# Optimization experiments

Hardware: AMD Instinct MI355X
Metric: run time of the kernel (lower is better)

The kernel has to match this reference:

```python
import jax, jax.numpy as jnp
import numpy as np

BATCH = 16384
INPUT_DIM = 1024
OUTPUT_DIM = 256
SCALES = 5  # pywt level = SCALES - 1

# pywt db4 decomposition low-pass filter (ascending index order)
DB4_LO = jnp.array([
    -0.010597401785069032, 0.0328830116668852, 0.030841381835560764,
    -0.18703481171909309, -0.027983769416859854, 0.6308807679298589,
    0.7148465705529157, 0.2303778133088965], dtype=jnp.float32)
# QMF: dec_hi[k] = (-1)^(k+1) * dec_lo[L-1-k]  (matches pywt sign convention)
_SIGNS = jnp.array([-1.0, 1.0, -1.0, 1.0, -1.0, 1.0, -1.0, 1.0], dtype=jnp.float32)
DB4_HI = DB4_LO[::-1] * _SIGNS


def _dwt_step(x, lo, hi):
    """Single-level pywt dwt with 'symmetric' mode along the last axis.
    x: [B, N] -> (cA, cD) each [B, floor((N+L-1)/2)]."""
    L = lo.shape[0]
    left = x[:, L - 2::-1]          # symmetric (half-point) left extension, L-1 samples
    right = x[:, -1:-L:-1]          # symmetric right extension, L-1 samples
    e = jnp.concatenate([left, x, right], axis=-1)[:, 1:]  # drop 1 to align odd-index downsample
    # convolution == correlation with reversed filter; stride-2 valid conv
    kern = jnp.stack([lo[::-1], hi[::-1]])[:, None, :]      # [2, 1, L]
    y = jax.lax.conv_general_dilated(
        e[:, None, :], kern, window_strides=(2,), padding='VALID',
        dimension_numbers=('NCW', 'OIW', 'NCW'))            # [B, 2, out_len]
    return y[:, 0], y[:, 1]


def _wavedec(x, level):
    """pywt.wavedec(x, 'db4', level) -> [cA_level, cD_level, ..., cD_1]."""
    ca = x
    details = []
    for _ in range(level):
        ca, cd = _dwt_step(ca, DB4_LO, DB4_HI)
        details.append(cd)
    return [ca] + details[::-1]


def setup_inputs() -> dict:
    key = jax.random.key(0)
    ks = jax.random.split(key, SCALES + 1)
    inp = {"x": jax.random.normal(ks[0], (BATCH, INPUT_DIM), dtype=jnp.float32)}
    for s in range(SCALES):
        inp[f"basis{s}"] = jax.random.normal(
            ks[s + 1], (INPUT_DIM // 2 ** s, OUTPUT_DIM), dtype=jnp.float32)
    return inp


def reference(x, basis0, basis1, basis2, basis3, basis4):
    bases = [basis0, basis1, basis2, basis3, basis4]
    coeffs = _wavedec(x, SCALES - 1)  # [cA4, cD4, cD3, cD2, cD1]
    out = jnp.zeros((x.shape[0], OUTPUT_DIM), dtype=x.dtype)
    for s in range(SCALES):
        m = min(coeffs[s].shape[-1], bases[s].shape[0])  # static; truncate to common length
        out = out + coeffs[s][:, :m] @ bases[s][:m]
    return out
```

## Files before the change

### kernel.cpp

```cpp
#include <hip/hip_runtime.h>
#include <stdint.h>

#define BATCH   16384
#define INDIM   1024
#define OUTDIM  256

constexpr int KP = 480;

typedef __attribute__((ext_vector_type(8))) short short8;
typedef __attribute__((ext_vector_type(4))) float f32x4;

__device__ __constant__ float LORc[8] = { 0.2303778133088965f,   0.7148465705529157f,
                                          0.6308807679298589f,  -0.027983769416859854f,
                                         -0.18703481171909309f,  0.030841381835560764f,
                                          0.0328830116668852f,  -0.010597401785069032f };
__device__ __constant__ float HIRc[8] = {-0.010597401785069032f, -0.0328830116668852f,
                                          0.030841381835560764f,  0.18703481171909309f,
                                         -0.027983769416859854f, -0.6308807679298589f,
                                          0.7148465705529157f,   -0.2303778133088965f };

__device__ __forceinline__ float symx(const float* __restrict__ in, int N, int t) {
    if (t < 0)  t = -1 - t;
    if (t >= N) t = 2 * N - 1 - t;
    return in[t];
}

__device__ __forceinline__ void dwt_level(const float* __restrict__ in, int N, int M,
                                          float* __restrict__ outA,
                                          float* __restrict__ outD, int nD, int lane) {
    for (int i = lane; i < M; i += 64) {
        const int base = 2 * i - 6;
        float a = 0.f, d = 0.f;
        if (base >= 0 && base + 7 < N) {
            #pragma unroll
            for (int k = 0; k < 8; ++k) {
                const float v = in[base + k];
                a = fmaf(v, LORc[k], a);
                d = fmaf(v, HIRc[k], d);
            }
        } else {
            #pragma unroll
            for (int k = 0; k < 8; ++k) {
                const float v = symx(in, N, base + k);
                a = fmaf(v, LORc[k], a);
                d = fmaf(v, HIRc[k], d);
            }
        }
        outA[i] = a;
        if (i < nD) outD[i] = d;
    }
}

__device__ __forceinline__ ushort f2bf_rne(float f) {
    union { float f; uint32_t u; } v; v.f = f;
    uint32_t r = v.u + 0x7fffu + ((v.u >> 16) & 1u);
    return (ushort)(r >> 16);
}
__device__ __forceinline__ float bf2f(ushort h) {
    union { uint32_t u; float f; } v; v.u = ((uint32_t)h) << 16;
    return v.f;
}

extern "C" __global__ __launch_bounds__(256)
void dwt_id(float* __restrict__ Wc)
{
    __shared__ float buf[4][1544];
    const int wid  = threadIdx.x >> 6;
    const int lane = threadIdx.x & 63;
    const int row  = blockIdx.x * 4 + wid;

    float* bufA = buf[wid];
    float* bufB = bufA + 1024;
    float* crow = Wc + (size_t)row * KP;

    for (int j = lane; j < 1024; j += 64) bufA[j] = (j == row) ? 1.f : 0.f;
    __syncthreads();
    dwt_level(bufA, 1024, 515, bufB, crow + 408, 64, lane);
    __syncthreads();
    dwt_level(bufB, 515, 261, bufA, crow + 280, 128, lane);
    __syncthreads();
    dwt_level(bufA, 261, 134, bufB, crow + 144, 134, lane);
    __syncthreads();
    dwt_level(bufB, 134, 70, crow, crow + 72, 70, lane);
    if (lane < 14) {
        const int padidx[14] = {70,71,142,143,278,279,472,473,474,475,476,477,478,479};
        crow[padidx[lane]] = 0.f;
    }
}

extern "C" __global__ __launch_bounds__(256)
void pack_b(const float* __restrict__ b0, const float* __restrict__ b1,
            const float* __restrict__ b2, const float* __restrict__ b3,
            const float* __restrict__ b4, float* __restrict__ Bp)
{
    const int k = blockIdx.x;
    const int n = threadIdx.x;
    float v = 0.f;
    if      (k < 70)              v = b0[(size_t)k * OUTDIM + n];
    else if (k >= 72  && k < 142) v = b1[(size_t)(k - 72)  * OUTDIM + n];
    else if (k >= 144 && k < 278) v = b2[(size_t)(k - 144) * OUTDIM + n];
    else if (k >= 280 && k < 408) v = b3[(size_t)(k - 280) * OUTDIM + n];
    else if (k >= 408 && k < 472) v = b4[(size_t)(k - 408) * OUTDIM + n];
    Bp[(size_t)k * OUTDIM + n] = v;
}

extern "C" __global__ __launch_bounds__(256)
void wgemm(const float* __restrict__ Wc, const float* __restrict__ Bp,
           float* __restrict__ W)
{
    __shared__ float wc[4][KP];
    const int tid = threadIdx.x;
    const int r0  = blockIdx.x * 4;

    #pragma unroll
    for (int r = 0; r < 4; ++r)
        for (int k = tid; k < KP; k += 256)
            wc[r][k] = Wc[(size_t)(r0 + r) * KP + k];
    __syncthreads();

    float acc[4] = {0.f, 0.f, 0.f, 0.f};
    for (int k = 0; k < KP; ++k) {
        const float b = Bp[(size_t)k * OUTDIM + tid];
        #pragma unroll
        for (int r = 0; r < 4; ++r) acc[r] = fmaf(wc[r][k], b, acc[r]);
    }
    #pragma unroll
    for (int r = 0; r < 4; ++r) W[(size_t)(r0 + r) * OUTDIM + tid] = acc[r];
}

extern "C" __global__ __launch_bounds__(256)
void bpack(const float* __restrict__ W, ushort* __restrict__ Bpk)
{
    const int slot  = blockIdx.x * 256 + threadIdx.x;
    const int chunk = slot >> 10;
    const int nf    = (slot >> 6) & 15;
    const int lane  = slot & 63;
    const int k     = chunk * 32 + (lane >> 4) * 8;
    const int n     = nf * 16 + (lane & 15);

    ushort hi[8], lo[8];
    #pragma unroll
    for (int j = 0; j < 8; ++j) {
        const float w = W[(size_t)(k + j) * OUTDIM + n];
        hi[j] = f2bf_rne(w);
        lo[j] = f2bf_rne(w - bf2f(hi[j]));
    }
    const size_t base = ((size_t)(chunk * 16 + nf) * 2) * 64 * 8 + (size_t)lane * 8;
    #pragma unroll
    for (int j = 0; j < 8; ++j) {
        Bpk[base + j]           = hi[j];
        Bpk[base + 512 + j]     = lo[j];
    }
}

extern "C" __global__ __launch_bounds__(512)
void wkan_mfma(const float* __restrict__ x, const ushort* __restrict__ Bpk,
               float* __restrict__ out)
{
    __shared__ ushort Ah[2][2][2][64][8];
    __shared__ ushort Bb[16][2][64][8];

    const int tid  = threadIdx.x;
    const int lane = tid & 63;
    const int wid  = tid >> 6;
    const int wm   = wid >> 2;
    const int wn   = wid & 3;
    const int row0 = blockIdx.x * 64;

    f32x4 acc[2][4];
    #pragma unroll
    for (int m = 0; m < 2; ++m)
        #pragma unroll
        for (int f = 0; f < 4; ++f) acc[m][f] = f32x4{0.f, 0.f, 0.f, 0.f};

    const int s_wm   = tid >> 7;
    const int s_mf   = (tid >> 6) & 1;
    const int s_lane = tid & 63;
    const int s_row  = s_wm * 32 + s_mf * 16 + (s_lane & 15);
    const int s_kg   = s_lane >> 4;
    const float* xrow = x + (size_t)(row0 + s_row) * INDIM + s_kg * 8;

    float4 af0, af1;
    uint4  bs0, bs1, bs2, bs3;

    {
        const ushort* bp = Bpk + (size_t)tid * 8;
        bs0 = *(const uint4*)(bp);
        bs1 = *(const uint4*)(bp + 4096);
        bs2 = *(const uint4*)(bp + 8192);
        bs3 = *(const uint4*)(bp + 12288);
        if (tid < 256) {
            af0 = *(const float4*)(xrow);
            af1 = *(const float4*)(xrow + 4);
        }
    }

    for (int c = 0; c < 32; ++c) {
        {
            ushort* bbf = &Bb[0][0][0][0] + (size_t)tid * 8;
            *(uint4*)(bbf)         = bs0;
            *(uint4*)(bbf + 4096)  = bs1;
            *(uint4*)(bbf + 8192)  = bs2;
            *(uint4*)(bbf + 12288) = bs3;
        }
        if (tid < 256) {
            const float a[8] = {af0.x, af0.y, af0.z, af0.w, af1.x, af1.y, af1.z, af1.w};
            uint32_t hw[4], lw[4];
            #pragma unroll
            for (int p = 0; p < 4; ++p) {
                const ushort h0 = f2bf_rne(a[2*p]),   h1 = f2bf_rne(a[2*p+1]);
                const ushort l0 = f2bf_rne(a[2*p]   - bf2f(h0));
                const ushort l1 = f2bf_rne(a[2*p+1] - bf2f(h1));
                hw[p] = (uint32_t)h0 | ((uint32_t)h1 << 16);
                lw[p] = (uint32_t)l0 | ((uint32_t)l1 << 16);
            }
            *(uint4*)&Ah[0][s_wm][s_mf][s_lane][0] = uint4{hw[0], hw[1], hw[2], hw[3]};
            *(uint4*)&Ah[1][s_wm][s_mf][s_lane][0] = uint4{lw[0], lw[1], lw[2], lw[3]};
        }
        __syncthreads();

        if (c < 31) {
            const ushort* bp = Bpk + (size_t)(c + 1) * 16384 + (size_t)tid * 8;
            bs0 = *(const uint4*)(bp);
            bs1 = *(const uint4*)(bp + 4096);
            bs2 = *(const uint4*)(bp + 8192);
            bs3 = *(const uint4*)(bp + 12288);
            if (tid < 256) {
                af0 = *(const float4*)(xrow + (c + 1) * 32);
                af1 = *(const float4*)(xrow + (c + 1) * 32 + 4);
            }
        }

        short8 afr[2][2];
        #pragma unroll
        for (int h = 0; h < 2; ++h)
            #pragma unroll
            for (int m = 0; m < 2; ++m)
                afr[h][m] = *(const short8*)&Ah[h][wm][m][lane][0];
        short8 bfr[4][2];
        #pragma unroll
        for (int f = 0; f < 4; ++f)
            #pragma unroll
            for (int h = 0; h < 2; ++h)
                bfr[f][h] = *(const short8*)&Bb[wn * 4 + f][h][lane][0];

        #pragma unroll
        for (int m = 0; m < 2; ++m)
            #pragma unroll
            for (int f = 0; f < 4; ++f) {
                acc[m][f] = __builtin_amdgcn_mfma_f32_16x16x32_bf16(afr[0][m], bfr[f][0], acc[m][f], 0, 0, 0);
                acc[m][f] = __builtin_amdgcn_mfma_f32_16x16x32_bf16(afr[0][m], bfr[f][1], acc[m][f], 0, 0, 0);
                acc[m][f] = __builtin_amdgcn_mfma_f32_16x16x32_bf16(afr[1][m], bfr[f][0], acc[m][f], 0, 0, 0);
            }
        __syncthreads();
    }

    #pragma unroll
    for (int m = 0; m < 2; ++m)
        #pragma unroll
        for (int f = 0; f < 4; ++f) {
            const int col = wn * 64 + f * 16 + (lane & 15);
            const int rowb = row0 + wm * 32 + m * 16 + (lane >> 4) * 4;
            #pragma unroll
            for (int r = 0; r < 4; ++r)
                out[(size_t)(rowb + r) * OUTDIM + col] = acc[m][f][r];
        }
}

constexpr int F_ROWS = 32;
constexpr int F_KP   = 472;

__device__ __forceinline__ void dwt_level_f(const float* __restrict__ in, int N, int M,
                                            float* __restrict__ outA,
                                            float* __restrict__ outD, int nD, int ht) {
    for (int i = ht; i < M; i += 128) {
        const int base = 2 * i - 6;
        float a = 0.f, d = 0.f;
        #pragma unroll
        for (int k = 0; k < 8; ++k) {
            const float v = symx(in, N, base + k);
            a = fmaf(v, LORc[k], a);
            d = fmaf(v, HIRc[k], d);
        }
        outA[i] = a;
        if (i < nD) outD[i] = d;
    }
}

extern "C" __global__ __launch_bounds__(256, 2)
void wkan_fused(const float* __restrict__ x,
                const float* __restrict__ b0, const float* __restrict__ b1,
                const float* __restrict__ b2, const float* __restrict__ b3,
                const float* __restrict__ b4,
                float* __restrict__ out)
{
    extern __shared__ float smem[];
    float* coef = smem;
    float* wbuf = smem + F_ROWS * F_KP;

    const int tid  = threadIdx.x;
    const int row0 = blockIdx.x * F_ROWS;

    for (int i = tid; i < F_ROWS * F_KP / 4; i += 256)
        ((float4*)coef)[i] = float4{0.f, 0.f, 0.f, 0.f};
    __syncthreads();

    const int slot = tid >> 7;
    const int ht   = tid & 127;
    float* bufA = wbuf + slot * 1544;
    float* bufB = bufA + 1024;

    for (int it = 0; it < F_ROWS / 2; ++it) {
        const int r = it * 2 + slot;
        float* crow = coef + r * F_KP;
        const float* xrow = x + (size_t)(row0 + r) * INDIM;
        ((float4*)bufA)[ht]       = ((const float4*)xrow)[ht];
        ((float4*)bufA)[ht + 128] = ((const float4*)xrow)[ht + 128];
        __syncthreads();
        dwt_level_f(bufA, 1024, 515, bufB, crow + 408, 64, ht);
        __syncthreads();
        dwt_level_f(bufB, 515, 261, bufA, crow + 280, 128, ht);
        __syncthreads();
        dwt_level_f(bufA, 261, 134, bufB, crow + 144, 134, ht);
        __syncthreads();
        dwt_level_f(bufB, 134, 70, crow, crow + 72, 70, ht);
        __syncthreads();
    }

    const int rg = tid >> 5;
    const int cg = tid & 31;
    float acc[4][8];
    #pragma unroll
    for (int r = 0; r < 4; ++r)
        #pragma unroll
        for (int c = 0; c < 8; ++c) acc[r][c] = 0.f;

    const float* Bs[5]  = { b0, b1, b2, b3, b4 };
    const int    off[5] = { 0, 72, 144, 280, 408 };
    const int    l4[5]  = { 72, 72, 136, 128, 64 };

    for (int s = 0; s < 5; ++s) {
        const float* __restrict__ B = Bs[s];
        const int o = off[s], L = l4[s];
        for (int k = 0; k < L; k += 4) {
            float4 bb[4][2];
            #pragma unroll
            for (int kk = 0; kk < 4; ++kk) {
                const float* bp = B + (size_t)(k + kk) * OUTDIM + cg * 8;
                bb[kk][0] = *(const float4*)(bp);
                bb[kk][1] = *(const float4*)(bp + 4);
            }
            #pragma unroll
            for (int rr = 0; rr < 4; ++rr) {
                const float4 c4 = *(const float4*)(coef + (rg * 4 + rr) * F_KP + o + k);
                const float cv[4] = { c4.x, c4.y, c4.z, c4.w };
                #pragma unroll
                for (int kk = 0; kk < 4; ++kk) {
                    acc[rr][0] = fmaf(cv[kk], bb[kk][0].x, acc[rr][0]);
                    acc[rr][1] = fmaf(cv[kk], bb[kk][0].y, acc[rr][1]);
                    acc[rr][2] = fmaf(cv[kk], bb[kk][0].z, acc[rr][2]);
                    acc[rr][3] = fmaf(cv[kk], bb[kk][0].w, acc[rr][3]);
                    acc[rr][4] = fmaf(cv[kk], bb[kk][1].x, acc[rr][4]);
                    acc[rr][5] = fmaf(cv[kk], bb[kk][1].y, acc[rr][5]);
                    acc[rr][6] = fmaf(cv[kk], bb[kk][1].z, acc[rr][6]);
                    acc[rr][7] = fmaf(cv[kk], bb[kk][1].w, acc[rr][7]);
                }
            }
        }
    }

    #pragma unroll
    for (int rr = 0; rr < 4; ++rr) {
        float* op = out + (size_t)(row0 + rg * 4 + rr) * OUTDIM + cg * 8;
        *(float4*)(op)     = float4{ acc[rr][0], acc[rr][1], acc[rr][2], acc[rr][3] };
        *(float4*)(op + 4) = float4{ acc[rr][4], acc[rr][5], acc[rr][6], acc[rr][7] };
    }
}

extern "C" void kernel_launch(void* const* d_in, const int* in_sizes, int n_in,
                              void* d_out, int out_size, void* d_ws, size_t ws_size,
                              hipStream_t stream) {
    const float* x  = (const float*)d_in[0];
    const float* b0 = (const float*)d_in[1];
    const float* b1 = (const float*)d_in[2];
    const float* b2 = (const float*)d_in[3];
    const float* b3 = (const float*)d_in[4];
    const float* b4 = (const float*)d_in[5];
    float* out = (float*)d_out;

    const size_t nWc  = (size_t)1024 * KP;
    const size_t nBp  = (size_t)KP * OUTDIM;
    const size_t nW   = (size_t)1024 * OUTDIM;
    const size_t nBpk = (size_t)1024 * OUTDIM * 2;
    const size_t need = (nWc + nBp + nW) * 4 + nBpk * 2;

    if (ws_size >= need) {
        float*  Wc  = (float*)d_ws;
        float*  Bp  = Wc + nWc;
        float*  W   = Bp + nBp;
        ushort* Bpk = (ushort*)(W + nW);

        hipLaunchKernelGGL(pack_b,  dim3(KP),   dim3(256), 0, stream, b0, b1, b2, b3, b4, Bp);
        hipLaunchKernelGGL(dwt_id,  dim3(256),  dim3(256), 0, stream, Wc);
        hipLaunchKernelGGL(wgemm,   dim3(256),  dim3(256), 0, stream, Wc, Bp, W);
        hipLaunchKernelGGL(bpack,   dim3(128),  dim3(256), 0, stream, W, Bpk);
        hipLaunchKernelGGL(wkan_mfma, dim3(BATCH / 64), dim3(512), 0, stream, x, Bpk, out);
    } else {
        const size_t shmem = (size_t)(F_ROWS * F_KP + 2 * 1544) * sizeof(float);
        hipLaunchKernelGGL(wkan_fused, dim3(BATCH / F_ROWS), dim3(256), shmem, stream,
                           x, b0, b1, b2, b3, b4, out);
    }
}
```

Before: 175.9 us.

## Fuse prep kernels and double-buffer split-N MFMA GEMM with 2D grid

Cuts the setup chain from four kernels to two: the DWT identity pass and the basis packing now share one launch, and the small weight GEMM is fused with the bf16 hi/lo split and pack. The main MFMA kernel splits the 256 output columns across two blocks on grid.y, which doubles the block count. It also double-buffers the A and B shared tiles so there is one barrier per k-chunk, and all threads now cooperatively split x into bf16 pairs. The cost is that each x tile is read and split twice, once per N-half. The launch bounds are also tightened for occupancy.

```diff
diff --git a/kernel.cpp b/kernel.cpp
--- a/kernel.cpp
+++ b/kernel.cpp
@@ -61,104 +61,103 @@
     return v.f;
 }
 
+__device__ __forceinline__ void split2(float a0, float a1, uint32_t& hw, uint32_t& lw) {
+    const uint32_t u0 = __float_as_uint(a0), u1 = __float_as_uint(a1);
+    const uint32_t r0 = u0 + 0x7fffu + ((u0 >> 16) & 1u);
+    const uint32_t r1 = u1 + 0x7fffu + ((u1 >> 16) & 1u);
+    hw = (r0 >> 16) | (r1 & 0xffff0000u);
+    const float l0 = a0 - __uint_as_float(r0 & 0xffff0000u);
+    const float l1 = a1 - __uint_as_float(r1 & 0xffff0000u);
+    const uint32_t v0 = __float_as_uint(l0), v1 = __float_as_uint(l1);
+    const uint32_t s0 = v0 + 0x7fffu + ((v0 >> 16) & 1u);
+    const uint32_t s1 = v1 + 0x7fffu + ((v1 >> 16) & 1u);
+    lw = (s0 >> 16) | (s1 & 0xffff0000u);
+}
+
 extern "C" __global__ __launch_bounds__(256)
-void dwt_id(float* __restrict__ Wc)
+void prep1(const float* __restrict__ b0, const float* __restrict__ b1,
+           const float* __restrict__ b2, const float* __restrict__ b3,
+           const float* __restrict__ b4,
+           float* __restrict__ Wc, float* __restrict__ Bp)
 {
     __shared__ float buf[4][1544];
-    const int wid  = threadIdx.x >> 6;
-    const int lane = threadIdx.x & 63;
-    const int row  = blockIdx.x * 4 + wid;
-
-    float* bufA = buf[wid];
-    float* bufB = bufA + 1024;
-    float* crow = Wc + (size_t)row * KP;
-
-    for (int j = lane; j < 1024; j += 64) bufA[j] = (j == row) ? 1.f : 0.f;
+    const int tid = threadIdx.x;
+    if (blockIdx.x < 256) {
+        const int wid  = tid >> 6;
+        const int lane = tid & 63;
+        const int row  = blockIdx.x * 4 + wid;
+        float* bufA = buf[wid];
+        float* bufB = bufA + 1024;
+        float* crow = Wc + (size_t)row * KP;
+        for (int j = lane; j < 1024; j += 64) bufA[j] = (j == row) ? 1.f : 0.f;
+        __syncthreads();
+        dwt_level(bufA, 1024, 515, bufB, crow + 408, 64, lane);
+        __syncthreads();
+        dwt_level(bufB, 515, 261, bufA, crow + 280, 128, lane);
+        __syncthreads();
+        dwt_level(bufA, 261, 134, bufB, crow + 144, 134, lane);
+        __syncthreads();
+        dwt_level(bufB, 134, 70, crow, crow + 72, 70, lane);
+        if (lane < 14) {
+            const int padidx[14] = {70,71,142,143,278,279,472,473,474,475,476,477,478,479};
+            crow[padidx[lane]] = 0.f;
+        }
+    } else {
+        const int k  = (blockIdx.x - 256) * 4 + (tid >> 6);
+        const int n0 = (tid & 63) * 4;
+        float4 v = float4{0.f, 0.f, 0.f, 0.f};
+        if      (k < 70)              v = *(const float4*)(b0 + (size_t)k * OUTDIM + n0);
+        else if (k >= 72  && k < 142) v = *(const float4*)(b1 + (size_t)(k - 72)  * OUTDIM + n0);
+        else if (k >= 144 && k < 278) v = *(const float4*)(b2 + (size_t)(k - 144) * OUTDIM + n0);
+        else if (k >= 280 && k < 408) v = *(const float4*)(b3 + (size_t)(k - 280) * OUTDIM + n0);
+        else if (k >= 408 && k < 472) v = *(const float4*)(b4 + (size_t)(k - 408) * OUTDIM + n0);
+        *(float4*)(Bp + (size_t)k * OUTDIM + n0) = v;
+    }
+}
+
+extern "C" __global__ __launch_bounds__(256)
+void prep2(const float* __restrict__ Wc, const float* __restrict__ Bp,
+           ushort* __restrict__ Bpk)
+{
+    __shared__ float wc[8][KP];
+    const int tid = threadIdx.x;
+    const int k0  = blockIdx.x * 8;
+    const int r   = tid >> 5;
+    for (int k = (tid & 31); k < KP; k += 32)
+        wc[r][k] = Wc[(size_t)(k0 + r) * KP + k];
     __syncthreads();
-    dwt_level(bufA, 1024, 515, bufB, crow + 408, 64, lane);
-    __syncthreads();
-    dwt_level(bufB, 515, 261, bufA, crow + 280, 128, lane);
-    __syncthreads();
-    dwt_level(bufA, 261, 134, bufB, crow + 144, 134, lane);
-    __syncthreads();
-    dwt_level(bufB, 134, 70, crow, crow + 72, 70, lane);
-    if (lane < 14) {
-        const int padidx[14] = {70,71,142,143,278,279,472,473,474,475,476,477,478,479};
-        crow[padidx[lane]] = 0.f;
-    }
-}
-
-extern "C" __global__ __launch_bounds__(256)
-void pack_b(const float* __restrict__ b0, const float* __restrict__ b1,
-            const float* __restrict__ b2, const float* __restrict__ b3,
-            const float* __restrict__ b4, float* __restrict__ Bp)
-{
-    const int k = blockIdx.x;
-    const int n = threadIdx.x;
-    float v = 0.f;
-    if      (k < 70)              v = b0[(size_t)k * OUTDIM + n];
-    else if (k >= 72  && k < 142) v = b1[(size_t)(k - 72)  * OUTDIM + n];
-    else if (k >= 144 && k < 278) v = b2[(size_t)(k - 144) * OUTDIM + n];
-    else if (k >= 280 && k < 408) v = b3[(size_t)(k - 280) * OUTDIM + n];
-    else if (k >= 408 && k < 472) v = b4[(size_t)(k - 408) * OUTDIM + n];
-    Bp[(size_t)k * OUTDIM + n] = v;
-}
-
-extern "C" __global__ __launch_bounds__(256)
-void wgemm(const float* __restrict__ Wc, const float* __restrict__ Bp,
-           float* __restrict__ W)
-{
-    __shared__ float wc[4][KP];
-    const int tid = threadIdx.x;
-    const int r0  = blockIdx.x * 4;
-
-    #pragma unroll
-    for (int r = 0; r < 4; ++r)
-        for (int k = tid; k < KP; k += 256)
-            wc[r][k] = Wc[(size_t)(r0 + r) * KP + k];
-    __syncthreads();
-
-    float acc[4] = {0.f, 0.f, 0.f, 0.f};
+
+    float acc[8] = {0,0,0,0,0,0,0,0};
     for (int k = 0; k < KP; ++k) {
         const float b = Bp[(size_t)k * OUTDIM + tid];
         #pragma unroll
-        for (int r = 0; r < 4; ++r) acc[r] = fmaf(wc[r][k], b, acc[r]);
-    }
-    #pragma unroll
-    for (int r = 0; r < 4; ++r) W[(size_t)(r0 + r) * OUTDIM + tid] = acc[r];
-}
-
-extern "C" __global__ __launch_bounds__(256)
-void bpack(const float* __restrict__ W, ushort* __restrict__ Bpk)
-{
-    const int slot  = blockIdx.x * 256 + threadIdx.x;
-    const int chunk = slot >> 10;
-    const int nf    = (slot >> 6) & 15;
-    const int lane  = slot & 63;
-    const int k     = chunk * 32 + (lane >> 4) * 8;
-    const int n     = nf * 16 + (lane & 15);
-
-    ushort hi[8], lo[8];
+        for (int j = 0; j < 8; ++j) acc[j] = fmaf(wc[j][k], b, acc[j]);
+    }
+
+    const int chunk = blockIdx.x >> 2, kg = blockIdx.x & 3;
+    const int nf = tid >> 4, ln = tid & 15;
+    const int lane = kg * 16 + ln;
+    ushort h[8], l[8];
     #pragma unroll
     for (int j = 0; j < 8; ++j) {
-        const float w = W[(size_t)(k + j) * OUTDIM + n];
-        hi[j] = f2bf_rne(w);
-        lo[j] = f2bf_rne(w - bf2f(hi[j]));
-    }
-    const size_t base = ((size_t)(chunk * 16 + nf) * 2) * 64 * 8 + (size_t)lane * 8;
-    #pragma unroll
-    for (int j = 0; j < 8; ++j) {
-        Bpk[base + j]           = hi[j];
-        Bpk[base + 512 + j]     = lo[j];
-    }
-}
-
-extern "C" __global__ __launch_bounds__(512)
+        h[j] = f2bf_rne(acc[j]);
+        l[j] = f2bf_rne(acc[j] - bf2f(h[j]));
+    }
+    const size_t base = ((size_t)(chunk * 16 + nf) * 2) * 512 + (size_t)lane * 8;
+    uint4 hv = { (uint32_t)h[0] | ((uint32_t)h[1] << 16), (uint32_t)h[2] | ((uint32_t)h[3] << 16),
+                 (uint32_t)h[4] | ((uint32_t)h[5] << 16), (uint32_t)h[6] | ((uint32_t)h[7] << 16) };
+    uint4 lv = { (uint32_t)l[0] | ((uint32_t)l[1] << 16), (uint32_t)l[2] | ((uint32_t)l[3] << 16),
+                 (uint32_t)l[4] | ((uint32_t)l[5] << 16), (uint32_t)l[6] | ((uint32_t)l[7] << 16) };
+    *(uint4*)(Bpk + base)       = hv;
+    *(uint4*)(Bpk + base + 512) = lv;
+}
+
+extern "C" __global__ __launch_bounds__(512, 4)
 void wkan_mfma(const float* __restrict__ x, const ushort* __restrict__ Bpk,
                float* __restrict__ out)
 {
-    __shared__ ushort Ah[2][2][2][64][8];
-    __shared__ ushort Bb[16][2][64][8];
+    __shared__ ushort Bb[2][8][2][64][8];
+    __shared__ ushort Ah[2][2][2][2][64][8];
 
     const int tid  = threadIdx.x;
     const int lane = tid & 63;
@@ -166,91 +165,82 @@
     const int wm   = wid >> 2;
     const int wn   = wid & 3;
     const int row0 = blockIdx.x * 64;
-
-    f32x4 acc[2][4];
+    const int nf0  = blockIdx.y * 8;
+
+    const int srow  = tid >> 3;
+    const int sk0   = (tid & 7) << 2;
+    const int slane = (sk0 >> 3) * 16 + (srow & 15);
+    const int sj0   = sk0 & 7;
+    const int swm   = srow >> 5, smf = (srow >> 4) & 1;
+
+    const float*  agp = x + (size_t)(row0 + srow) * INDIM + sk0;
+    const ushort* bgp = Bpk + (size_t)nf0 * 1024 + (size_t)tid * 8;
+
+    f32x4 acc[2][2];
     #pragma unroll
     for (int m = 0; m < 2; ++m)
         #pragma unroll
-        for (int f = 0; f < 4; ++f) acc[m][f] = f32x4{0.f, 0.f, 0.f, 0.f};
-
-    const int s_wm   = tid >> 7;
-    const int s_mf   = (tid >> 6) & 1;
-    const int s_lane = tid & 63;
-    const int s_row  = s_wm * 32 + s_mf * 16 + (s_lane & 15);
-    const int s_kg   = s_lane >> 4;
-    const float* xrow = x + (size_t)(row0 + s_row) * INDIM + s_kg * 8;
-
-    float4 af0, af1;
-    uint4  bs0, bs1, bs2, bs3;
-
+        for (int f = 0; f < 2; ++f) acc[m][f] = f32x4{0.f, 0.f, 0.f, 0.f};
+
+    float4 av; uint4 bv0, bv1;
+
+    av  = *(const float4*)(agp);
+    bv0 = *(const uint4*)(bgp);
+    bv1 = *(const uint4*)(bgp + 4096);
     {
-        const ushort* bp = Bpk + (size_t)tid * 8;
-        bs0 = *(const uint4*)(bp);
-        bs1 = *(const uint4*)(bp + 4096);
-        bs2 = *(const uint4*)(bp + 8192);
-        bs3 = *(const uint4*)(bp + 12288);
-        if (tid < 256) {
-            af0 = *(const float4*)(xrow);
-            af1 = *(const float4*)(xrow + 4);
-        }
-    }
+        uint32_t hw0, lw0, hw1, lw1;
+        split2(av.x, av.y, hw0, lw0);
+        split2(av.z, av.w, hw1, lw1);
+        *(uint2*)&Ah[0][swm][smf][0][slane][sj0] = uint2{hw0, hw1};
+        *(uint2*)&Ah[0][swm][smf][1][slane][sj0] = uint2{lw0, lw1};
+        ushort* bd = &Bb[0][0][0][0][0] + (size_t)tid * 8;
+        *(uint4*)bd          = bv0;
+        *(uint4*)(bd + 4096) = bv1;
+    }
+    av  = *(const float4*)(agp + 32);
+    bv0 = *(const uint4*)(bgp + 16384);
+    bv1 = *(const uint4*)(bgp + 16384 + 4096);
+    __syncthreads();
 
     for (int c = 0; c < 32; ++c) {
-        {
-            ushort* bbf = &Bb[0][0][0][0] + (size_t)tid * 8;
-            *(uint4*)(bbf)         = bs0;
-            *(uint4*)(bbf + 4096)  = bs1;
-            *(uint4*)(bbf + 8192)  = bs2;
-            *(uint4*)(bbf + 12288) = bs3;
-        }
-        if (tid < 256) {
-            const float a[8] = {af0.x, af0.y, af0.z, af0.w, af1.x, af1.y, af1.z, af1.w};
-            uint32_t hw[4], lw[4];
-            #pragma unroll
-            for (int p = 0; p < 4; ++p) {
-                const ushort h0 = f2bf_rne(a[2*p]),   h1 = f2bf_rne(a[2*p+1]);
-                const ushort l0 = f2bf_rne(a[2*p]   - bf2f(h0));
-                const ushort l1 = f2bf_rne(a[2*p+1] - bf2f(h1));
-                hw[p] = (uint32_t)h0 | ((uint32_t)h1 << 16);
-                lw[p] = (uint32_t)l0 | ((uint32_t)l1 << 16);
-            }
-            *(uint4*)&Ah[0][s_wm][s_mf][s_lane][0] = uint4{hw[0], hw[1], hw[2], hw[3]};
-            *(uint4*)&Ah[1][s_wm][s_mf][s_lane][0] = uint4{lw[0], lw[1], lw[2], lw[3]};
-        }
-        __syncthreads();
+        const int cur = c & 1, nx = cur ^ 1;
 
         if (c < 31) {
-            const ushort* bp = Bpk + (size_t)(c + 1) * 16384 + (size_t)tid * 8;
-            bs0 = *(const uint4*)(bp);
-            bs1 = *(const uint4*)(bp + 4096);
-            bs2 = *(const uint4*)(bp + 8192);
-            bs3 = *(const uint4*)(bp + 12288);
-            if (tid < 256) {
-                af0 = *(const float4*)(xrow + (c + 1) * 32);
-                af1 = *(const float4*)(xrow + (c + 1) * 32 + 4);
-            }
-        }
-
-        short8 afr[2][2];
-        #pragma unroll
-        for (int h = 0; h < 2; ++h)
-            #pragma unroll
-            for (int m = 0; m < 2; ++m)
-                afr[h][m] = *(const short8*)&Ah[h][wm][m][lane][0];
-        short8 bfr[4][2];
-        #pragma unroll
-        for (int f = 0; f < 4; ++f)
+            uint32_t hw0, lw0, hw1, lw1;
+            split2(av.x, av.y, hw0, lw0);
+            split2(av.z, av.w, hw1, lw1);
+            *(uint2*)&Ah[nx][swm][smf][0][slane][sj0] = uint2{hw0, hw1};
+            *(uint2*)&Ah[nx][swm][smf][1][slane][sj0] = uint2{lw0, lw1};
+            ushort* bd = &Bb[nx][0][0][0][0] + (size_t)tid * 8;
+            *(uint4*)bd          = bv0;
+            *(uint4*)(bd + 4096) = bv1;
+        }
+        if (c < 30) {
+            av = *(const float4*)(agp + (size_t)(c + 2) * 32);
+            const ushort* bs = bgp + (size_t)(c + 2) * 16384;
+            bv0 = *(const uint4*)bs;
+            bv1 = *(const uint4*)(bs + 4096);
+        }
+
+        short8 afr[2][2], bfr[2][2];
+        #pragma unroll
+        for (int m = 0; m < 2; ++m)
             #pragma unroll
             for (int h = 0; h < 2; ++h)
-                bfr[f][h] = *(const short8*)&Bb[wn * 4 + f][h][lane][0];
+                afr[m][h] = *(const short8*)&Ah[cur][wm][m][h][lane][0];
+        #pragma unroll
+        for (int f = 0; f < 2; ++f)
+            #pragma unroll
+            for (int h = 0; h < 2; ++h)
+                bfr[f][h] = *(const short8*)&Bb[cur][wn * 2 + f][h][lane][0];
 
         #pragma unroll
         for (int m = 0; m < 2; ++m)
             #pragma unroll
-            for (int f = 0; f < 4; ++f) {
-                acc[m][f] = __builtin_amdgcn_mfma_f32_16x16x32_bf16(afr[0][m], bfr[f][0], acc[m][f], 0, 0, 0);
-                acc[m][f] = __builtin_amdgcn_mfma_f32_16x16x32_bf16(afr[0][m], bfr[f][1], acc[m][f], 0, 0, 0);
-                acc[m][f] = __builtin_amdgcn_mfma_f32_16x16x32_bf16(afr[1][m], bfr[f][0], acc[m][f], 0, 0, 0);
+            for (int f = 0; f < 2; ++f) {
+                acc[m][f] = __builtin_amdgcn_mfma_f32_16x16x32_bf16(afr[m][0], bfr[f][0], acc[m][f], 0, 0, 0);
+                acc[m][f] = __builtin_amdgcn_mfma_f32_16x16x32_bf16(afr[m][0], bfr[f][1], acc[m][f], 0, 0, 0);
+                acc[m][f] = __builtin_amdgcn_mfma_f32_16x16x32_bf16(afr[m][1], bfr[f][0], acc[m][f], 0, 0, 0);
             }
         __syncthreads();
     }
@@ -258,8 +248,8 @@
     #pragma unroll
     for (int m = 0; m < 2; ++m)
         #pragma unroll
-        for (int f = 0; f < 4; ++f) {
-            const int col = wn * 64 + f * 16 + (lane & 15);
+        for (int f = 0; f < 2; ++f) {
+            const int col  = nf0 * 16 + wn * 32 + f * 16 + (lane & 15);
             const int rowb = row0 + wm * 32 + m * 16 + (lane >> 4) * 4;
             #pragma unroll
             for (int r = 0; r < 4; ++r)
@@ -390,21 +380,19 @@
 
     const size_t nWc  = (size_t)1024 * KP;
     const size_t nBp  = (size_t)KP * OUTDIM;
-    const size_t nW   = (size_t)1024 * OUTDIM;
     const size_t nBpk = (size_t)1024 * OUTDIM * 2;
-    const size_t need = (nWc + nBp + nW) * 4 + nBpk * 2;
+    const size_t need = (nWc + nBp) * 4 + nBpk * 2;
 
     if (ws_size >= need) {
         float*  Wc  = (float*)d_ws;
         float*  Bp  = Wc + nWc;
-        float*  W   = Bp + nBp;
-        ushort* Bpk = (ushort*)(W + nW);
-
-        hipLaunchKernelGGL(pack_b,  dim3(KP),   dim3(256), 0, stream, b0, b1, b2, b3, b4, Bp);
-        hipLaunchKernelGGL(dwt_id,  dim3(256),  dim3(256), 0, stream, Wc);
-        hipLaunchKernelGGL(wgemm,   dim3(256),  dim3(256), 0, stream, Wc, Bp, W);
-        hipLaunchKernelGGL(bpack,   dim3(128),  dim3(256), 0, stream, W, Bpk);
-        hipLaunchKernelGGL(wkan_mfma, dim3(BATCH / 64), dim3(512), 0, stream, x, Bpk, out);
+        ushort* Bpk = (ushort*)(Bp + nBp);
+
+        hipLaunchKernelGGL(prep1, dim3(376), dim3(256), 0, stream,
+                           b0, b1, b2, b3, b4, Wc, Bp);
+        hipLaunchKernelGGL(prep2, dim3(128), dim3(256), 0, stream, Wc, Bp, Bpk);
+        hipLaunchKernelGGL(wkan_mfma, dim3(BATCH / 64, 2), dim3(512), 0, stream,
+                           x, Bpk, out);
     } else {
         const size_t shmem = (size_t)(F_ROWS * F_KP + 2 * 1544) * sizeof(float);
         hipLaunchKernelGGL(wkan_fused, dim3(BATCH / F_ROWS), dim3(256), shmem, stream,
```

Result: faster. 160.9 us (-8.5%).
